# Performance work log

Hardware: AMD Instinct MI355X
Metric: run time of the kernel (lower is better)

## Reference

```python
import jax, jax.numpy as jnp
import numpy as np

B, H, W, CIN, COUT, KH, KW = 16, 64, 64, 256, 256, 3, 3


def setup_inputs() -> dict:
    key = jax.random.key(0)
    k1, k2, k3 = jax.random.split(key, 3)
    x = jax.random.normal(k1, (B, H, W, CIN), dtype=jnp.float32)
    style = jax.random.normal(k2, (B, CIN), dtype=jnp.float32)
    # glorot-ish scale for the base kernel
    kernel = jax.random.normal(k3, (KH, KW, CIN, COUT), dtype=jnp.float32) * 0.05
    return {"x": x, "style": style, "kernel": kernel}


def reference(x, style, kernel):
    b = x.shape[0]
    cout = kernel.shape[-1]
    # Modulate: per-sample weights [B, kh, kw, Cin, Cout]
    w = kernel[None] * (style[:, None, None, :, None] + 1.0)
    # Demodulate: L2 normalize over (kh, kw, Cin) per (sample, out-channel)
    w = w / jnp.sqrt(jnp.sum(jnp.square(w), axis=(1, 2, 3), keepdims=True) + 1e-8)
    # Batch-as-groups grouped conv: x -> [1, B*Cin, H, W]
    xg = jnp.transpose(x, (0, 3, 1, 2)).reshape(1, -1, x.shape[1], x.shape[2])
    # w -> [kh, kw, Cin, B*Cout]
    wg = jnp.transpose(w, (1, 2, 3, 0, 4)).reshape(w.shape[1], w.shape[2], w.shape[3], -1)
    y = jax.lax.conv_general_dilated(
        xg, wg,
        window_strides=(1, 1),
        padding='SAME',
        dimension_numbers=('NCHW', 'HWIO', 'NCHW'),
        feature_group_count=b,
    )
    # [1, B*Cout, H, W] -> [B, H, W, Cout]
    y = y.reshape(b, cout, y.shape[2], y.shape[3])
    return jnp.transpose(y, (0, 2, 3, 1))
```

## Files before the change

### kernel.cpp

```cpp
#include <hip/hip_runtime.h>


#define HH 64
#define WW 64
#define CI 256
#define CO 256
#define KTOT 2304
#define CIPITCH 40
#define XCOLS 66

typedef float    f32x4 __attribute__((ext_vector_type(4)));
typedef _Float16 f16x8 __attribute__((ext_vector_type(8)));
typedef __fp16   fp16x2 __attribute__((ext_vector_type(2)));

__device__ __forceinline__ unsigned pk2(float a, float b) {
    fp16x2 h = __builtin_amdgcn_cvt_pkrtz(a, b);
    return __builtin_bit_cast(unsigned, h);
}

__global__ __launch_bounds__(256) void prep(
    const float* __restrict__ kern,
    const float* __restrict__ style,
    ushort* __restrict__ Wt2,
    float* __restrict__ scale2)
{
    __shared__ ushort tile[64][65];
    __shared__ float  sqt[64][65];
    __shared__ float  st2l[16][64];

    const int kt = blockIdx.x >> 2;
    const int ct = blockIdx.x & 3;
    const int k0 = kt * 64, c0 = ct * 64;
    const int ci0 = k0 & 255;
    const int tid = threadIdx.x;
    const int r = tid >> 2, q = tid & 3;

    #pragma unroll
    for (int p = 0; p < 4; ++p) {
        const int i = p * 256 + tid;
        const int bb = i >> 6, rr = i & 63;
        const float s = style[bb * CI + ci0 + rr] + 1.0f;
        st2l[bb][rr] = s * s;
    }

    const float* src = kern + (size_t)(k0 + r) * CO + c0 + q * 16;
    #pragma unroll
    for (int j = 0; j < 16; ++j) {
        const float v = src[j];
        _Float16 h = (_Float16)v;
        tile[q * 16 + j][r] = __builtin_bit_cast(unsigned short, h);
        sqt[r][q * 16 + j] = v * v;
    }
    __syncthreads();

    const int co_w = c0 + r;
    #pragma unroll
    for (int j = 0; j < 16; ++j) {
        const int k   = k0 + q * 16 + j;
        const int t9  = k >> 8;
        const int rem = k & 255;
        const int cc  = rem >> 5;
        const int fq  = (rem >> 3) & 3;
        const int e   = k & 7;
        Wt2[((((size_t)cc * 9 + t9) * 4 + fq) * 256 + co_w) * 8 + e] =
            tile[r][q * 16 + j];
    }

    const int co = tid & 63;
    const int bq = tid >> 6;
    float acc[4] = {0.f, 0.f, 0.f, 0.f};
    #pragma unroll 4
    for (int rr = 0; rr < 64; ++rr) {
        const float s = sqt[rr][co];
        #pragma unroll
        for (int bb = 0; bb < 4; ++bb)
            acc[bb] += s * st2l[bq * 4 + bb][rr];
    }
    #pragma unroll
    for (int bb = 0; bb < 4; ++bb)
        atomicAdd(&scale2[(bq * 4 + bb) * CO + c0 + co], acc[bb]);
}

__global__ __launch_bounds__(256) void gemm_conv(
    const float* __restrict__ x,
    const ushort* __restrict__ Wt2,
    const float* __restrict__ style,
    const float* __restrict__ scale2,
    float* __restrict__ y)
{
    __shared__ __align__(16) ushort xs[4 * XCOLS * CIPITCH];
    __shared__ __align__(16) ushort bs[3 * 4096];
    __shared__ float s_style[CI];

    const int tid  = threadIdx.x;
    const int lane = tid & 63;
    const int wave = tid >> 6;

    const int mtile = blockIdx.x >> 1;
    const int n0    = (blockIdx.x & 1) * 128;
    const int p0    = mtile * 128;
    const int b     = p0 >> 12;
    const int h0    = (p0 >> 6) & 63;

    s_style[tid] = style[b * CI + tid] + 1.0f;

    const int wm = (wave & 1) * 64;
    const int wn = (wave >> 1) * 64;
    const int fr = lane & 15;
    const int fq = lane >> 4;
    const int xlane = fr * CIPITCH + fq * 8;

    auto issue_tile = [&](int cn, int t9n, int bufn) {
        const ushort* gb = Wt2 + ((size_t)((cn * 9 + t9n) * 4) * 256 + n0) * 8;
        #pragma unroll
        for (int p = 0; p < 2; ++p) {
            const int task = p * 256 + tid;
            const ushort* g = gb + (size_t)(((task >> 7) << 8) + (task & 127)) * 8;
            const ushort* l = bs + bufn * 4096 + (p * 256 + (tid & ~63)) * 8;
            __builtin_amdgcn_global_load_lds(
                (const __attribute__((address_space(1))) void*)g,
                (__attribute__((address_space(3))) void*)l,
                16, 0, 0);
        }
    };

    f32x4 acc[4][4] = {};

    issue_tile(0, 0, 0);
    issue_tile(0, 1, 1);

    for (int c = 0; c < 8; ++c) {
        #pragma unroll
        for (int t9 = 0; t9 < 9; ++t9) {
            asm volatile("s_waitcnt vmcnt(2) lgkmcnt(0)" ::: "memory");
            __builtin_amdgcn_s_barrier();

            if (t9 == 0) {
                #pragma unroll
                for (int p = 0; p < 9; ++p) {
                    const int task = p * 256 + tid;
                    if (task < 2112) {
                        const int rowcol = task >> 3;
                        const int chunk  = task & 7;
                        const int row = rowcol / XCOLS;
                        const int col = rowcol - row * XCOLS;
                        const int rg = h0 - 1 + row;
                        const int cg = col - 1;
                        f32x4 v = {0.f, 0.f, 0.f, 0.f};
                        if ((unsigned)rg < 64u && (unsigned)cg < 64u)
                            v = *(const f32x4*)(x + ((size_t)((b * HH + rg) * WW + cg)) * CI
                                                  + c * 32 + chunk * 4);
                        const f32x4 st = *(const f32x4*)(s_style + c * 32 + chunk * 4);
                        const f32x4 m = v * st;
                        uint2 u;
                        u.x = pk2(m.x, m.y);
                        u.y = pk2(m.z, m.w);
                        *(uint2*)(xs + rowcol * CIPITCH + chunk * 4) = u;
                    }
                }
                asm volatile("s_waitcnt lgkmcnt(0)" ::: "memory");
                __builtin_amdgcn_s_barrier();
            }

            {
                const int tn  = t9 + 2;
                const int t9n = (tn >= 9) ? tn - 9 : tn;
                if (t9 < 7) {
                    issue_tile(c, t9n, t9n % 3);
                } else if (c < 7) {
                    issue_tile(c + 1, t9n, t9n % 3);
                }
            }

            {
                const int buf = t9 % 3;
                const int dh  = t9 / 3;
                const int dw  = t9 - dh * 3;

                f16x8 af[4], bf[4];
                #pragma unroll
                for (int i = 0; i < 4; ++i) {
                    const int mb   = wm + i * 16;
                    const int mrow = (mb >> 6) + dh;
                    const int mcol = (mb & 63) + dw;
                    af[i] = *(const f16x8*)(xs + (mrow * XCOLS + mcol) * CIPITCH + xlane);
                }
                #pragma unroll
                for (int j = 0; j < 4; ++j)
                    bf[j] = *(const f16x8*)(bs + buf * 4096 + fq * 1024
                                            + (wn + j * 16 + fr) * 8);
                #pragma unroll
                for (int i = 0; i < 4; ++i)
                    #pragma unroll
                    for (int j = 0; j < 4; ++j)
                        acc[i][j] = __builtin_amdgcn_mfma_f32_16x16x32_f16(
                            af[i], bf[j], acc[i][j], 0, 0, 0);
            }
        }
    }

    float sc[4];
    #pragma unroll
    for (int j = 0; j < 4; ++j)
        sc[j] = __frsqrt_rn(scale2[b * CO + n0 + wn + j * 16 + fr] + 1e-8f);
    #pragma unroll
    for (int i = 0; i < 4; ++i) {
        const int m_base = p0 + wm + i * 16 + fq * 4;
        #pragma unroll
        for (int j = 0; j < 4; ++j) {
            float* yp = y + (size_t)m_base * CO + n0 + wn + j * 16 + fr;
            #pragma unroll
            for (int r = 0; r < 4; ++r)
                yp[(size_t)r * CO] = acc[i][j][r] * sc[j];
        }
    }
}

extern "C" void kernel_launch(void* const* d_in, const int* in_sizes, int n_in,
                              void* d_out, int out_size, void* d_ws, size_t ws_size,
                              hipStream_t stream) {
    const float* x     = (const float*)d_in[0];
    const float* style = (const float*)d_in[1];
    const float* kern  = (const float*)d_in[2];
    float* out = (float*)d_out;

    float*  scale2 = (float*)d_ws;
    ushort* Wt2    = (ushort*)((char*)d_ws + 16384);

    hipMemsetAsync(scale2, 0, 16 * CO * sizeof(float), stream);
    prep<<<144, 256, 0, stream>>>(kern, style, Wt2, scale2);
    gemm_conv<<<512 * 2, 256, 0, stream>>>(x, Wt2, style, scale2, out);
}
```

Measured before the change: 225.7 us.

## Precompute padded fp16 modulated input and load A fragments directly from global

Result: slower. 333.7 us (+47.9%).

```diff
diff --git a/kernel.cpp b/kernel.cpp
--- a/kernel.cpp
+++ b/kernel.cpp
@@ -5,7 +5,7 @@
 #define WW 64
 #define CI 256
 #define CO 256
-#define KTOT 2304
+#define XP 66
 #define CIPITCH 40
 #define XCOLS 66
 
@@ -81,7 +81,159 @@
         atomicAdd(&scale2[(bq * 4 + bb) * CO + c0 + co], acc[bb]);
 }
 
-__global__ __launch_bounds__(256) void gemm_conv(
+__global__ __launch_bounds__(256) void xmod_k(
+    const float* __restrict__ x,
+    const float* __restrict__ style,
+    ushort* __restrict__ Xm)
+{
+    const int b  = blockIdx.x / XP;
+    const int hh = blockIdx.x - b * XP;
+    const int tid = threadIdx.x;
+    ushort* dst = Xm + ((size_t)(b * XP + hh)) * XP * CI;
+
+    if (hh == 0 || hh == XP - 1) {
+        const uint4 z = {0, 0, 0, 0};
+        #pragma unroll
+        for (int p = 0; p < 9; ++p) {
+            const int t = p * 256 + tid;
+            if (t < 2112) *(uint4*)(dst + t * 8) = z;
+        }
+        return;
+    }
+
+    const int l = tid & 63;
+    const int q = tid >> 6;
+    const int ci0 = l * 4;
+    const int rg = hh - 1;
+
+    f32x4 st = *(const f32x4*)(style + b * CI + ci0);
+    st.x += 1.f; st.y += 1.f; st.z += 1.f; st.w += 1.f;
+
+    const float* srow = x + ((size_t)(b * HH + rg)) * WW * CI + ci0;
+    #pragma unroll
+    for (int k = 0; k < 17; ++k) {
+        const int cc = q + 4 * k;
+        if (cc < XP) {
+            uint2 u = {0, 0};
+            if (cc >= 1 && cc <= WW) {
+                const f32x4 v = *(const f32x4*)(srow + (size_t)(cc - 1) * CI);
+                const f32x4 m = v * st;
+                u.x = pk2(m.x, m.y);
+                u.y = pk2(m.z, m.w);
+            }
+            *(uint2*)(dst + cc * CI + ci0) = u;
+        }
+    }
+}
+
+__global__ __launch_bounds__(256) void gemm_xm(
+    const ushort* __restrict__ Xm,
+    const ushort* __restrict__ Wt2,
+    const float* __restrict__ scale2,
+    float* __restrict__ y)
+{
+    __shared__ __align__(16) ushort bs[3 * 4096];
+
+    const int tid  = threadIdx.x;
+    const int lane = tid & 63;
+    const int wave = tid >> 6;
+
+    const int mtile = blockIdx.x >> 1;
+    const int n0    = (blockIdx.x & 1) * 128;
+    const int p0    = mtile * 128;
+    const int b     = p0 >> 12;
+    const int h0    = (p0 >> 6) & 63;
+
+    const int wm = (wave & 1) * 64;
+    const int wn = (wave >> 1) * 64;
+    const int fr = lane & 15;
+    const int fq = lane >> 4;
+
+    const ushort* xb = Xm + (size_t)b * XP * XP * CI;
+    unsigned offA[4];
+    #pragma unroll
+    for (int i = 0; i < 4; ++i) {
+        const int mb = wm + i * 16;
+        const int R0 = h0 + (mb >> 6);
+        const int C0 = (mb & 63) + fr;
+        offA[i] = (unsigned)((R0 * XP + C0) * CI + fq * 8);
+    }
+
+    auto issue_tile = [&](int cn, int t9n, int bufn) {
+        const ushort* gb = Wt2 + ((size_t)((cn * 9 + t9n) * 4) * 256 + n0) * 8;
+        #pragma unroll
+        for (int p = 0; p < 2; ++p) {
+            const int task = p * 256 + tid;
+            const ushort* g = gb + (size_t)(((task >> 7) << 8) + (task & 127)) * 8;
+            const ushort* l = bs + bufn * 4096 + (p * 256 + (tid & ~63)) * 8;
+            __builtin_amdgcn_global_load_lds(
+                (const __attribute__((address_space(1))) void*)g,
+                (__attribute__((address_space(3))) void*)l,
+                16, 0, 0);
+        }
+    };
+
+    f32x4 acc[4][4] = {};
+
+    issue_tile(0, 0, 0);
+    issue_tile(0, 1, 1);
+
+    for (int c = 0; c < 8; ++c) {
+        #pragma unroll
+        for (int t9 = 0; t9 < 9; ++t9) {
+            if (c == 7 && t9 == 8)
+                asm volatile("s_waitcnt vmcnt(0) lgkmcnt(0)" ::: "memory");
+            else
+                asm volatile("s_waitcnt vmcnt(2) lgkmcnt(0)" ::: "memory");
+            __builtin_amdgcn_s_barrier();
+
+            {
+                const int t2 = (t9 + 2 >= 9) ? t9 + 2 - 9 : t9 + 2;
+                const int c2 = (t9 >= 7) ? c + 1 : c;
+                if (c2 < 8) issue_tile(c2, t2, (t9 + 2) % 3);
+            }
+
+            const int dh = t9 / 3;
+            const int dw = t9 - dh * 3;
+            const int buf = t9 % 3;
+
+            f16x8 af[4], bf[4];
+            #pragma unroll
+            for (int i = 0; i < 4; ++i)
+                af[i] = *(const f16x8*)(xb + offA[i] + (dh * XP + dw) * CI);
+            #pragma unroll
+            for (int j = 0; j < 4; ++j)
+                bf[j] = *(const f16x8*)(bs + buf * 4096 + fq * 1024
+                                        + (wn + j * 16 + fr) * 8);
+            #pragma unroll
+            for (int i = 0; i < 4; ++i)
+                #pragma unroll
+                for (int j = 0; j < 4; ++j)
+                    acc[i][j] = __builtin_amdgcn_mfma_f32_16x16x32_f16(
+                        af[i], bf[j], acc[i][j], 0, 0, 0);
+        }
+        #pragma unroll
+        for (int i = 0; i < 4; ++i) offA[i] += 32;
+    }
+
+    float sc[4];
+    #pragma unroll
+    for (int j = 0; j < 4; ++j)
+        sc[j] = __frsqrt_rn(scale2[b * CO + n0 + wn + j * 16 + fr] + 1e-8f);
+    #pragma unroll
+    for (int i = 0; i < 4; ++i) {
+        const int m_base = p0 + wm + i * 16 + fq * 4;
+        #pragma unroll
+        for (int j = 0; j < 4; ++j) {
+            float* yp = y + (size_t)m_base * CO + n0 + wn + j * 16 + fr;
+            #pragma unroll
+            for (int r = 0; r < 4; ++r)
+                yp[(size_t)r * CO] = acc[i][j][r] * sc[j];
+        }
+    }
+}
+
+__global__ __launch_bounds__(256) void gemm_lds(
     const float* __restrict__ x,
     const ushort* __restrict__ Wt2,
     const float* __restrict__ style,
@@ -163,39 +315,33 @@
             }
 
             {
-                const int tn  = t9 + 2;
-                const int t9n = (tn >= 9) ? tn - 9 : tn;
-                if (t9 < 7) {
-                    issue_tile(c, t9n, t9n % 3);
-                } else if (c < 7) {
-                    issue_tile(c + 1, t9n, t9n % 3);
-                }
-            }
-
-            {
-                const int buf = t9 % 3;
-                const int dh  = t9 / 3;
-                const int dw  = t9 - dh * 3;
-
-                f16x8 af[4], bf[4];
-                #pragma unroll
-                for (int i = 0; i < 4; ++i) {
-                    const int mb   = wm + i * 16;
-                    const int mrow = (mb >> 6) + dh;
-                    const int mcol = (mb & 63) + dw;
-                    af[i] = *(const f16x8*)(xs + (mrow * XCOLS + mcol) * CIPITCH + xlane);
-                }
+                const int t2 = (t9 + 2 >= 9) ? t9 + 2 - 9 : t9 + 2;
+                const int c2 = (t9 >= 7) ? c + 1 : c;
+                if (c2 < 8) issue_tile(c2, t2, (t9 + 2) % 3);
+            }
+
+            const int buf = t9 % 3;
+            const int dh  = t9 / 3;
+            const int dw  = t9 - dh * 3;
+
+            f16x8 af[4], bf[4];
+            #pragma unroll
+            for (int i = 0; i < 4; ++i) {
+                const int mb   = wm + i * 16;
+                const int mrow = (mb >> 6) + dh;
+                const int mcol = (mb & 63) + dw;
+                af[i] = *(const f16x8*)(xs + (mrow * XCOLS + mcol) * CIPITCH + xlane);
+            }
+            #pragma unroll
+            for (int j = 0; j < 4; ++j)
+                bf[j] = *(const f16x8*)(bs + buf * 4096 + fq * 1024
+                                        + (wn + j * 16 + fr) * 8);
+            #pragma unroll
+            for (int i = 0; i < 4; ++i)
                 #pragma unroll
                 for (int j = 0; j < 4; ++j)
-                    bf[j] = *(const f16x8*)(bs + buf * 4096 + fq * 1024
-                                            + (wn + j * 16 + fr) * 8);
-                #pragma unroll
-                for (int i = 0; i < 4; ++i)
-                    #pragma unroll
-                    for (int j = 0; j < 4; ++j)
-                        acc[i][j] = __builtin_amdgcn_mfma_f32_16x16x32_f16(
-                            af[i], bf[j], acc[i][j], 0, 0, 0);
-            }
+                    acc[i][j] = __builtin_amdgcn_mfma_f32_16x16x32_f16(
+                        af[i], bf[j], acc[i][j], 0, 0, 0);
         }
     }
 
@@ -227,7 +373,17 @@
     float*  scale2 = (float*)d_ws;
     ushort* Wt2    = (ushort*)((char*)d_ws + 16384);
 
+    const size_t xm_off  = 16384 + 1179648;
+    const size_t xm_size = (size_t)16 * XP * XP * CI * 2;
+
     hipMemsetAsync(scale2, 0, 16 * CO * sizeof(float), stream);
     prep<<<144, 256, 0, stream>>>(kern, style, Wt2, scale2);
-    gemm_conv<<<512 * 2, 256, 0, stream>>>(x, Wt2, style, scale2, out);
-}
+
+    if (ws_size >= xm_off + xm_size) {
+        ushort* Xm = (ushort*)((char*)d_ws + xm_off);
+        xmod_k<<<16 * XP, 256, 0, stream>>>(x, style, Xm);
+        gemm_xm<<<512 * 2, 256, 0, stream>>>(Xm, Wt2, scale2, out);
+    } else {
+        gemm_lds<<<512 * 2, 256, 0, stream>>>(x, Wt2, style, scale2, out);
+    }
+}
```
